# Optimization experiments

Hardware: AMD Instinct MI355X
Metric: run time of the kernel (lower is better)

The kernel has to match this reference:

```python
import jax, jax.numpy as jnp
import numpy as np

B, CIN, H, W = 4, 256, 128, 128   # x1/x2 each [B, CIN, H, W]
C2 = 2 * CIN                       # 512, channels after concat
CQK = CIN // 8                     # 32, query/key channels


def setup_inputs() -> dict:
    key = jax.random.key(0)
    ks = jax.random.split(key, 12)
    s = 0.02
    return {
        "x1": jax.random.normal(ks[0], (B, CIN, H, W), jnp.float32),
        "x2": jax.random.normal(ks[1], (B, CIN, H, W), jnp.float32),
        # 1x1 convs as [out,in] matrices + bias
        "Wq": jax.random.normal(ks[2], (CQK, C2), jnp.float32) * s,
        "bq": jnp.zeros((CQK,), jnp.float32),
        "Wk": jax.random.normal(ks[3], (CQK, C2), jnp.float32) * s,
        "bk": jnp.zeros((CQK,), jnp.float32),
        "Wv": jax.random.normal(ks[4], (C2, C2), jnp.float32) * s,
        "bv": jnp.zeros((C2,), jnp.float32),
        "Wm": jax.random.normal(ks[5], (C2, C2), jnp.float32) * s,
        "bm": jnp.zeros((C2,), jnp.float32),
        "gamma": jnp.zeros((1,), jnp.float32),
    }


def _conv1x1(w, b, x):
    # x: [b,c,h,w] -> [b,o,h,w]
    return jnp.einsum('oc,bchw->bohw', w, x) + b[None, :, None, None]


def reference(x1, x2, Wq, bq, Wk, bk, Wv, bv, Wm, bm, gamma):
    b, _, h, w = x1.shape
    x = jnp.concatenate([x1, x2], axis=1)          # [b, 2C, h, w]
    q = _conv1x1(Wq, bq, x)                        # [b, cqk, h, w]
    k = _conv1x1(Wk, bk, x)                        # [b, cqk, h, w]
    v = _conv1x1(Wv, bv, x)                        # [b, 2C, h, w]

    # column (H-axis) energy: [b, h_q, w, h_k], diagonal h_q==h_k masked to -inf
    energy_H = jnp.einsum('bciw,bcjw->biwj', q, k)
    diag = jnp.eye(h, dtype=bool)[None, :, None, :]
    energy_H = jnp.where(diag, -jnp.inf, energy_H)
    # row (W-axis) energy: [b, h, w_q, w_k]
    energy_W = jnp.einsum('bchi,bchj->bhij', q, k)

    concate = jax.nn.softmax(jnp.concatenate([energy_H, energy_W], axis=3), axis=3)
    att_H = concate[..., :h]                       # [b, h_q, w, h_k]
    att_W = concate[..., h:]                       # [b, h, w_q, w_k]

    out_H = jnp.einsum('bcjw,biwj->bciw', v, att_H)  # [b, 2C, h, w]
    out_W = jnp.einsum('bchj,bhij->bchi', v, att_W)  # [b, 2C, h, w]

    out = gamma[0] * (out_H + out_W) + x
    out = _conv1x1(Wm, bm, out)                    # [b, 2C, h, w]
    out = out.reshape(b, 2, C2 // 2, h, w).transpose(1, 0, 2, 3, 4)
    return out
```

## Files before the change

### kernel.cpp

```cpp
#include <hip/hip_runtime.h>
#include <cstdint>

#define HW 16384
#define HH 128
#define WW 128
#define C2 512
#define CQK 32
#define NB_TOT 4

typedef unsigned short u16;
typedef unsigned int u32;

using bf16x8 = __attribute__((ext_vector_type(8))) short;
using f32x4  = __attribute__((ext_vector_type(4))) float;

__device__ __forceinline__ float us2f(u16 u) { return __uint_as_float(((u32)u) << 16); }
__device__ __forceinline__ u16 f2us(float f) {
    u32 u = __float_as_uint(f);
    u = u + 0x7fffu + ((u >> 16) & 1u);
    return (u16)(u >> 16);
}
__device__ __forceinline__ u32 pack2(float a, float b) {
    return (u32)f2us(a) | ((u32)f2us(b) << 16);
}
__device__ __forceinline__ void unpack8(uint4 p, float* f) {
    u32 a[4] = {p.x, p.y, p.z, p.w};
#pragma unroll
    for (int q = 0; q < 4; ++q) {
        f[q * 2 + 0] = __uint_as_float(a[q] << 16);
        f[q * 2 + 1] = __uint_as_float(a[q] & 0xffff0000u);
    }
}
union U8 { uint4 v; u16 s[8]; };

__device__ __forceinline__ void gl_lds16(const void* g, const void* lds) {
    __builtin_amdgcn_global_load_lds(
        (const __attribute__((address_space(1))) unsigned int*)g,
        (__attribute__((address_space(3))) unsigned int*)lds, 16, 0, 0);
}

__global__ __launch_bounds__(256) void convert_weights(
    const float* __restrict__ Wq, const float* __restrict__ Wk,
    const float* __restrict__ Wv, const float* __restrict__ Wm,
    u16* __restrict__ Wall)
{
    int id = blockIdx.x * 256 + threadIdx.x;
    if (id >= 1088 * 128) return;
    int row = id >> 7, q4 = id & 127;
    const float* src;
    if (row < 32) src = Wq + (size_t)row * 512;
    else if (row < 64) src = Wk + (size_t)(row - 32) * 512;
    else if (row < 576) src = Wv + (size_t)(row - 64) * 512;
    else src = Wm + (size_t)(row - 576) * 512;
    float4 v = *reinterpret_cast<const float4*>(src + q4 * 4);
    alignas(8) u16 h[4] = {f2us(v.x), f2us(v.y), f2us(v.z), f2us(v.w)};
    *reinterpret_cast<uint2*>(Wall + (size_t)row * 512 + q4 * 4) =
        *reinterpret_cast<uint2*>(h);
}

__global__ __launch_bounds__(512) void conv_final(
    const u16* __restrict__ Wmb, const float* __restrict__ bm,
    const float* __restrict__ x1, const float* __restrict__ x2,
    const u16* __restrict__ y, float* __restrict__ out,
    int b0, const float* __restrict__ gamma)
{
    __shared__ u16 As[2][512 * 64];
    __shared__ u32 Ps[128 * 36];
    const int t = threadIdx.x, lane = t & 63, wid = t >> 6;
    const int bz = blockIdx.z, bg = b0 + bz;
    const int p0 = blockIdx.x * 128;
    const int l15 = lane & 15, l16 = lane >> 4;
    const bool useY = (gamma[0] != 0.f);
    const int pcol = t & 15, cpair = t >> 4;
    const u16* yb = y + (size_t)bz * C2 * HW;

    f32x4 acc[4][8];
#pragma unroll
    for (int i = 0; i < 4; ++i)
#pragma unroll
        for (int j = 0; j < 8; ++j) acc[i][j] = (f32x4)0.f;

    u32 xr[16];

    auto stageW = [&](int k0, int b) {
#pragma unroll
        for (int it = 0; it < 8; ++it) {
            int sflat = it * 512 + t;
            int m = sflat >> 3, slot = sflat & 7;
            int ck = slot ^ (m & 7);
            gl_lds16(Wmb + (size_t)m * 512 + k0 + ck * 8, &As[b][sflat * 8]);
        }
    };
    auto loadX = [&](int k0) {
        const int ce = k0 + cpair * 2;
        if (useY) {
            const u16* s0 = yb + (size_t)ce * HW + p0;
            const u16* s1 = s0 + HW;
#pragma unroll
            for (int i = 0; i < 8; ++i) {
                int p = pcol + i * 16;
                xr[i] = s0[p]; xr[8 + i] = s1[p];
            }
        } else {
            const float* s0 = (ce < 256) ? x1 + ((size_t)bg * 256 + ce) * HW + p0
                                         : x2 + ((size_t)bg * 256 + ce - 256) * HW + p0;
            const float* s1 = s0 + HW;
#pragma unroll
            for (int i = 0; i < 8; ++i) {
                int p = pcol + i * 16;
                xr[i] = __float_as_uint(s0[p]);
                xr[8 + i] = __float_as_uint(s1[p]);
            }
        }
    };
    auto writeX = [&]() {
#pragma unroll
        for (int i = 0; i < 8; ++i) {
            int p = pcol + i * 16;
            u32 d = useY ? (xr[i] | (xr[8 + i] << 16))
                         : pack2(__uint_as_float(xr[i]), __uint_as_float(xr[8 + i]));
            Ps[p * 36 + cpair] = d;
        }
    };

    stageW(0, 0);
    loadX(0);
    writeX();
    __syncthreads();

    for (int k = 0; k < 8; ++k) {
        const int cb = k & 1;
        if (k < 7) {
            stageW((k + 1) * 64, cb ^ 1);
            loadX((k + 1) * 64);
        }
#pragma unroll
        for (int kk = 0; kk < 2; ++kk) {
            bf16x8 af[4];
#pragma unroll
            for (int mi = 0; mi < 4; ++mi) {
                int row = wid * 64 + mi * 16 + l15;
                int slot = (kk * 4 + l16) ^ (row & 7);
                af[mi] = *(const bf16x8*)&As[cb][row * 64 + slot * 8];
            }
#pragma unroll
            for (int ni = 0; ni < 8; ++ni) {
                bf16x8 bq = *(const bf16x8*)((const u16*)&Ps[(ni * 16 + l15) * 36 + kk * 16 + l16 * 4]);
#pragma unroll
                for (int mi = 0; mi < 4; ++mi)
                    acc[mi][ni] = __builtin_amdgcn_mfma_f32_16x16x32_bf16(
                        af[mi], bq, acc[mi][ni], 0, 0, 0);
            }
        }
        __syncthreads();
        if (k < 7) {
            writeX();
            __syncthreads();
        }
    }
#pragma unroll
    for (int mi = 0; mi < 4; ++mi)
#pragma unroll
        for (int ni = 0; ni < 8; ++ni) {
            const int p = p0 + ni * 16 + l15;
#pragma unroll
            for (int r = 0; r < 4; ++r) {
                const int m = wid * 64 + mi * 16 + l16 * 4 + r;
                out[(((size_t)(m >> 8) * NB_TOT + bg) * 256 + (m & 255)) * HW + p] =
                    acc[mi][ni][r] + bm[m];
            }
        }
}

__global__ __launch_bounds__(256) void transpose_x(
    const float* __restrict__ x1, const float* __restrict__ x2,
    u16* __restrict__ xT, int b0, const float* __restrict__ gamma)
{
    if (gamma[0] == 0.f) return;
    __shared__ u16 tile[32][33];
    const int bz = blockIdx.z, bg = b0 + bz;
    const int p0 = blockIdx.x * 32;
    const int tx = threadIdx.x, ty = threadIdx.y;
    for (int cy = 0; cy < 16; ++cy) {
        const int c0 = cy * 32;
#pragma unroll
        for (int u = 0; u < 4; ++u) {
            int c = c0 + ty + u * 8;
            const float* xs = (c < 256) ? x1 + ((size_t)bg * 256 + c) * HW
                                        : x2 + ((size_t)bg * 256 + (c - 256)) * HW;
            tile[ty + u * 8][tx] = f2us(xs[p0 + tx]);
        }
        __syncthreads();
#pragma unroll
        for (int u = 0; u < 4; ++u) {
            int p = p0 + ty + u * 8;
            xT[((size_t)bz * HW + p) * 512 + c0 + tx] = tile[tx][ty + u * 8];
        }
        __syncthreads();
    }
}

template <int BM, int MODE>
__global__ __launch_bounds__(256) void conv_mfma(
    const u16* __restrict__ Wb, const float* __restrict__ bias0,
    const float* __restrict__ bias1, const u16* __restrict__ xT,
    float* __restrict__ oQ, float* __restrict__ oK,
    u16* __restrict__ oV, int b0, const float* __restrict__ gamma)
{
    if (gamma[0] == 0.f) return;
    constexpr int FM = BM / 32;
    __shared__ u16 As[BM * 64];
    __shared__ u16 Ps[128 * 64];
    const int t = threadIdx.x, lane = t & 63, wid = t >> 6;
    const int wr = wid >> 1, wc = wid & 1;
    const int bz = blockIdx.z;
    const int p0 = blockIdx.x * 128, m0 = blockIdx.y * BM;
    const u16* xTb = xT + (size_t)bz * HW * 512;
    const int l15 = lane & 15, l16 = lane >> 4;

    f32x4 acc[FM][4];
#pragma unroll
    for (int i = 0; i < FM; ++i)
#pragma unroll
        for (int j = 0; j < 4; ++j) acc[i][j] = (f32x4)0.f;

    for (int c0 = 0; c0 < 512; c0 += 64) {
#pragma unroll
        for (int it = 0; it < BM / 32; ++it) {
            int flat = it * 256 + t;
            int row = flat >> 3, part = flat & 7;
            gl_lds16(Wb + (size_t)(m0 + row) * 512 + c0 + part * 8,
                     As + (it * 256 + wid * 64) * 8);
        }
#pragma unroll
        for (int it = 0; it < 4; ++it) {
            int flat = it * 256 + t;
            int row = flat >> 3, part = flat & 7;
            gl_lds16(xTb + (size_t)(p0 + row) * 512 + c0 + part * 8,
                     Ps + (it * 256 + wid * 64) * 8);
        }
        __syncthreads();
#pragma unroll
        for (int kk = 0; kk < 2; ++kk) {
            bf16x8 af[FM], bfr[4];
#pragma unroll
            for (int mi = 0; mi < FM; ++mi)
                af[mi] = *(const bf16x8*)&As[(wr * (BM / 2) + mi * 16 + l15) * 64 + kk * 32 + l16 * 8];
#pragma unroll
            for (int ni = 0; ni < 4; ++ni)
                bfr[ni] = *(const bf16x8*)&Ps[(wc * 64 + ni * 16 + l15) * 64 + kk * 32 + l16 * 8];
#pragma unroll
            for (int mi = 0; mi < FM; ++mi)
#pragma unroll
                for (int ni = 0; ni < 4; ++ni)
                    acc[mi][ni] = __builtin_amdgcn_mfma_f32_16x16x32_bf16(
                        af[mi], bfr[ni], acc[mi][ni], 0, 0, 0);
        }
        __syncthreads();
    }
#pragma unroll
    for (int mi = 0; mi < FM; ++mi)
#pragma unroll
        for (int ni = 0; ni < 4; ++ni) {
            const int p = p0 + wc * 64 + ni * 16 + l15;
#pragma unroll
            for (int r = 0; r < 4; ++r) {
                const int m = m0 + wr * (BM / 2) + mi * 16 + l16 * 4 + r;
                float val = acc[mi][ni][r];
                if (MODE == 0) {
                    if (m < 32) {
                        val += bias0[m];
                        oQ[((size_t)bz * 32 + m) * HW + p] = val;
                    } else {
                        val += bias1[m - 32];
                        oK[((size_t)bz * 32 + (m - 32)) * HW + p] = val;
                    }
                } else {
                    val += bias0[m];
                    oV[((size_t)bz * 512 + m) * HW + p] = f2us(val);
                }
            }
        }
}

__global__ __launch_bounds__(256) void transpose_bf16(
    const u16* __restrict__ in, u16* __restrict__ out,
    const float* __restrict__ gamma)
{
    if (gamma[0] == 0.f) return;
    __shared__ u16 tile[32][33];
    const int x0 = blockIdx.x * 32, y0 = blockIdx.y * 32;
    const int tx = threadIdx.x, ty = threadIdx.y;
    for (int pp = 0; pp < 16; ++pp) {
        const int plane = blockIdx.z * 16 + pp;
        const u16* ip = in + (size_t)plane * HW;
        u16* op = out + (size_t)plane * HW;
#pragma unroll
        for (int u = 0; u < 4; ++u)
            tile[ty + u * 8][tx] = ip[(size_t)(y0 + ty + u * 8) * WW + x0 + tx];
        __syncthreads();
#pragma unroll
        for (int u = 0; u < 4; ++u)
            op[(size_t)(x0 + ty + u * 8) * HH + y0 + tx] = tile[tx][ty + u * 8];
        __syncthreads();
    }
}

__global__ __launch_bounds__(256) void energy_h_kernel(
    const float* __restrict__ q, const float* __restrict__ k,
    u16* __restrict__ EHt, const float* __restrict__ gamma)
{
    if (gamma[0] == 0.f) return;
    const int w = blockIdx.x, bz = blockIdx.y, t = threadIdx.x;
    __shared__ float qc[32][128];
    __shared__ float kc[32][128];
    __shared__ u16 es[128][128];
    for (int it = 0; it < 16; ++it) {
        int idx = it * 256 + t;
        int c = idx >> 7, j = idx & 127;
        qc[c][j] = q[((size_t)bz * CQK + c) * HW + j * WW + w];
        kc[c][j] = k[((size_t)bz * CQK + c) * HW + j * WW + w];
    }
    __syncthreads();
    const int i = t & 127, half = t >> 7, j0 = half * 64;
    float qi[32];
#pragma unroll
    for (int c = 0; c < 32; ++c) qi[c] = qc[c][i];
    for (int j = j0; j < j0 + 64; ++j) {
        float acc = 0.f;
#pragma unroll
        for (int c = 0; c < 32; ++c) acc += qi[c] * kc[c][j];
        es[i][j] = f2us(i == j ? -1e30f : acc);
    }
    __syncthreads();
    u16* dst = EHt + ((size_t)bz * WW + w) * HW;
    for (int it = 0; it < 8; ++it) {
        int ii = it * 16 + (t >> 4), jj = (t & 15) * 8;
        *reinterpret_cast<uint4*>(&dst[(size_t)ii * HH + jj]) =
            *reinterpret_cast<const uint4*>(&es[ii][jj]);
    }
}

__global__ __launch_bounds__(256) void ew_softmax_ow_kernel(
    const float* __restrict__ q, const float* __restrict__ k,
    const u16* __restrict__ v, u16* __restrict__ EHt,
    u16* __restrict__ oW, const float* __restrict__ gamma)
{
    if (gamma[0] == 0.f) return;
    const int r = blockIdx.x, bz = blockIdx.y, t = threadIdx.x;
    __shared__ float qr[32][128];
    __shared__ float kr[32][128];
    __shared__ u16 ewT[128][136];
    __shared__ u16 vstageT[128][40];
    __shared__ float invA[128];
    __shared__ float red[2][2][128];

    for (int it = 0; it < 16; ++it) {
        int idx = it * 256 + t, c = idx >> 7, j = idx & 127;
        qr[c][j] = q[((size_t)bz * CQK + c) * HW + r * WW + j];
        kr[c][j] = k[((size_t)bz * CQK + c) * HW + r * WW + j];
    }
    __syncthreads();
    const int i = t & 127, half = t >> 7, j0 = half * 64;
    {
        float qi[32];
#pragma unroll
        for (int c = 0; c < 32; ++c) qi[c] = qr[c][i];
        for (int j = j0; j < j0 + 64; ++j) {
            float acc = 0.f;
#pragma unroll
            for (int c = 0; c < 32; ++c) acc += qi[c] * kr[c][j];
            ewT[j][i] = f2us(acc);
        }
    }
    __syncthreads();
    float eh[64];
    u16* ehrow = EHt + (((size_t)bz * WW + i) * HH + r) * HH + j0;
#pragma unroll
    for (int uq = 0; uq < 8; ++uq) {
        uint4 pk = *reinterpret_cast<const uint4*>(ehrow + uq * 8);
        unpack8(pk, eh + uq * 8);
    }
    float m = -3e38f;
#pragma unroll
    for (int u = 0; u < 64; ++u) m = fmaxf(m, eh[u]);
    for (int j = j0; j < j0 + 64; ++j) m = fmaxf(m, us2f(ewT[j][i]));
    red[0][half][i] = m;
    __syncthreads();
    m = fmaxf(red[0][0][i], red[0][1][i]);
    float s = 0.f;
#pragma unroll
    for (int u = 0; u < 64; ++u) { float e = __expf(eh[u] - m); eh[u] = e; s += e; }
    for (int j = j0; j < j0 + 64; ++j) {
        float e = __expf(us2f(ewT[j][i]) - m);
        ewT[j][i] = f2us(e);
        s += e;
    }
    red[1][half][i] = s;
    __syncthreads();
    const float inv = 1.f / (red[1][0][i] + red[1][1][i]);
    if (half == 0) invA[i] = inv;
#pragma unroll
    for (int uq = 0; uq < 8; ++uq) {
        alignas(16) u16 tmp[8];
#pragma unroll
        for (int e = 0; e < 8; ++e) tmp[e] = f2us(eh[uq * 8 + e] * inv);
        *reinterpret_cast<uint4*>(ehrow + uq * 8) = *reinterpret_cast<uint4*>(tmp);
    }
    const int cg = half;
    for (int c0 = 0; c0 < C2; c0 += 32) {
        __syncthreads();
        for (int it = 0; it < 16; ++it) {
            int idx = it * 256 + t, cc = idx >> 7, j = idx & 127;
            vstageT[j][cc] = v[((size_t)bz * C2 + c0 + cc) * HW + r * WW + j];
        }
        __syncthreads();
        float acc[16] = {};
        for (int j = 0; j < 128; ++j) {
            float a = us2f(ewT[j][i]);
            uint4 pq0 = *reinterpret_cast<const uint4*>(&vstageT[j][cg * 16]);
            uint4 pq1 = *reinterpret_cast<const uint4*>(&vstageT[j][cg * 16 + 8]);
            float vv[16];
            unpack8(pq0, vv);
            unpack8(pq1, vv + 8);
#pragma unroll
            for (int u = 0; u < 16; ++u) acc[u] += a * vv[u];
        }
        const float scale = invA[i];
#pragma unroll
        for (int u = 0; u < 16; ++u) {
            int c = c0 + cg * 16 + u;
            oW[((size_t)bz * C2 + c) * HW + r * WW + i] = f2us(acc[u] * scale);
        }
    }
}

__global__ __launch_bounds__(256) void apply_h_kernel(
    const u16* __restrict__ EHt, const u16* __restrict__ vT,
    u16* __restrict__ oHT, const float* __restrict__ gamma)
{
    if (gamma[0] == 0.f) return;
    const int w = blockIdx.x, bz = blockIdx.y, t = threadIdx.x;
    __shared__ u16 aT[128][136];
    __shared__ u16 vstageT[128][40];
    const u16* src = EHt + ((size_t)bz * WW + w) * HW;
    for (int it = 0; it < 8; ++it) {
        int oct = it * 256 + t;
        int ii = oct >> 4, jj = (oct & 15) * 8;
        U8 uu;
        uu.v = *reinterpret_cast<const uint4*>(src + (size_t)ii * HH + jj);
#pragma unroll
        for (int e = 0; e < 8; ++e) aT[jj + e][ii] = uu.s[e];
    }
    const int i = t & 127, cg = t >> 7;
    for (int c0 = 0; c0 < C2; c0 += 32) {
        __syncthreads();
        for (int it = 0; it < 16; ++it) {
            int idx = it * 256 + t, cc = idx >> 7, j = idx & 127;
            vstageT[j][cc] = vT[((size_t)bz * C2 + c0 + cc) * HW + w * HH + j];
        }
        __syncthreads();
        float acc[16] = {};
        for (int j = 0; j < 128; ++j) {
            float a = us2f(aT[j][i]);
            uint4 pq0 = *reinterpret_cast<const uint4*>(&vstageT[j][cg * 16]);
            uint4 pq1 = *reinterpret_cast<const uint4*>(&vstageT[j][cg * 16 + 8]);
            float vv[16];
            unpack8(pq0, vv);
            unpack8(pq1, vv + 8);
#pragma unroll
            for (int u = 0; u < 16; ++u) acc[u] += a * vv[u];
        }
#pragma unroll
        for (int u = 0; u < 16; ++u) {
            int c = c0 + cg * 16 + u;
            oHT[((size_t)bz * C2 + c) * HW + w * HH + i] = f2us(acc[u]);
        }
    }
}

__global__ __launch_bounds__(256) void merge_transpose_kernel(
    const u16* __restrict__ oHT, const u16* __restrict__ oW,
    const float* __restrict__ x1, const float* __restrict__ x2,
    const float* __restrict__ gamma, u16* __restrict__ y, int b0)
{
    const float g = gamma[0];
    if (g == 0.f) return;
    __shared__ float tile[32][33];
    const int w0 = blockIdx.x * 32, i0 = blockIdx.y * 32;
    const int tx = threadIdx.x, ty = threadIdx.y;
    for (int pp = 0; pp < 16; ++pp) {
        const int idx = blockIdx.z * 16 + pp;
        const int c = idx & 511, bz = idx >> 9;
        const int bg = b0 + bz;
        const u16* ih = oHT + ((size_t)bz * C2 + c) * HW;
#pragma unroll
        for (int u = 0; u < 4; ++u)
            tile[ty + u * 8][tx] = us2f(ih[(size_t)(w0 + ty + u * 8) * HH + i0 + tx]);
        __syncthreads();
        const float* xs = (c < 256) ? (x1 + ((size_t)bg * 256 + c) * HW)
                                    : (x2 + ((size_t)bg * 256 + (c - 256)) * HW);
        const u16* ow = oW + ((size_t)bz * C2 + c) * HW;
        u16* yy = y + ((size_t)bz * C2 + c) * HW;
#pragma unroll
        for (int u = 0; u < 4; ++u) {
            int i = i0 + ty + u * 8, w = w0 + tx;
            float oh = tile[tx][ty + u * 8];
            float val = g * (oh + us2f(ow[(size_t)i * WW + w])) + xs[(size_t)i * WW + w];
            yy[(size_t)i * WW + w] = f2us(val);
        }
        __syncthreads();
    }
}

extern "C" void kernel_launch(void* const* d_in, const int* in_sizes, int n_in,
                              void* d_out, int out_size, void* d_ws, size_t ws_size,
                              hipStream_t stream)
{
    const float* x1 = (const float*)d_in[0];
    const float* x2 = (const float*)d_in[1];
    const float* Wq = (const float*)d_in[2];
    const float* bq = (const float*)d_in[3];
    const float* Wk = (const float*)d_in[4];
    const float* bk = (const float*)d_in[5];
    const float* Wv = (const float*)d_in[6];
    const float* bv = (const float*)d_in[7];
    const float* Wm = (const float*)d_in[8];
    const float* bm = (const float*)d_in[9];
    const float* gamma = (const float*)d_in[10];
    float* out = (float*)d_out;

    auto algn = [](size_t v) { return (v + 255) & ~(size_t)255; };
    const size_t wallSz = algn((size_t)1088 * 512 * 2);
    auto need = [&](int nb) -> size_t {
        size_t s = wallSz;
        s += algn((size_t)nb * HW * 512 * 2);
        s += 2 * algn((size_t)nb * 32 * HW * 4);
        s += algn((size_t)nb * C2 * HW * 2);
        s += algn((size_t)nb * C2 * HW * 2);
        s += algn((size_t)nb * WW * HW * 2);
        s += algn((size_t)nb * C2 * HW * 2);
        s += algn((size_t)nb * C2 * HW * 2);
        return s;
    };
    const int nb = (ws_size >= need(4)) ? 4 : (ws_size >= need(2)) ? 2 : 1;

    char* base = (char*)d_ws;
    u16* Wall = (u16*)base; base += wallSz;
    const u16* Wqk = Wall;
    const u16* Wvb = Wall + (size_t)64 * 512;
    const u16* Wmb = Wall + (size_t)576 * 512;

    convert_weights<<<(1088 * 128 + 255) / 256, 256, 0, stream>>>(Wq, Wk, Wv, Wm, Wall);

    for (int b0 = 0; b0 < NB_TOT; b0 += nb) {
        char* p = base;
        u16* xT   = (u16*)p;   p += algn((size_t)nb * HW * 512 * 2);
        float* q  = (float*)p; p += algn((size_t)nb * 32 * HW * 4);
        float* kk = (float*)p; p += algn((size_t)nb * 32 * HW * 4);
        u16* v    = (u16*)p;   p += algn((size_t)nb * C2 * HW * 2);
        u16* vT   = (u16*)p;   p += algn((size_t)nb * C2 * HW * 2);
        u16* EHt  = (u16*)p;   p += algn((size_t)nb * WW * HW * 2);
        u16* oW   = (u16*)p;   p += algn((size_t)nb * C2 * HW * 2);
        u16* oHT  = (u16*)p;   p += algn((size_t)nb * C2 * HW * 2);
        u16* y    = vT;

        transpose_x<<<dim3(HW / 32, 1, nb), dim3(32, 8), 0, stream>>>(
            x1, x2, xT, b0, gamma);
        conv_mfma<64, 0><<<dim3(HW / 128, 1, nb), 256, 0, stream>>>(
            Wqk, bq, bk, xT, q, kk, nullptr, b0, gamma);
        conv_mfma<128, 1><<<dim3(HW / 128, 4, nb), 256, 0, stream>>>(
            Wvb, bv, nullptr, xT, nullptr, nullptr, v, b0, gamma);
        transpose_bf16<<<dim3(4, 4, nb * 32), dim3(32, 8), 0, stream>>>(v, vT, gamma);
        energy_h_kernel<<<dim3(WW, nb), 256, 0, stream>>>(q, kk, EHt, gamma);
        ew_softmax_ow_kernel<<<dim3(HH, nb), 256, 0, stream>>>(q, kk, v, EHt, oW, gamma);
        apply_h_kernel<<<dim3(WW, nb), 256, 0, stream>>>(EHt, vT, oHT, gamma);
        merge_transpose_kernel<<<dim3(4, 4, nb * 32), dim3(32, 8), 0, stream>>>(
            oHT, oW, x1, x2, gamma, y, b0);
        conv_final<<<dim3(HW / 128, 1, nb), 512, 0, stream>>>(
            Wmb, bm, x1, x2, y, out, b0, gamma);
    }
}
```

Before: 87.62 us.

## Vectorize conv_final X loads, relax barrier, skip unused weight conversion when gamma is zero

conv_final's X loader now maps 32 lanes to channel pairs and 8 lanes to pixel groups, so each thread issues 16-byte vector loads instead of scattered scalar loads. The X load is issued before the weight staging, and the trailing __syncthreads is replaced by a raw s_barrier plus sched_barrier, so the outstanding global loads are not drained before the LDS write. convert_weights skips converting Wq/Wk/Wv when gamma is zero, because the attention branch is not consumed then. The relaxed barrier depends on the LDS write being ordered correctly without a full waitcnt, and the gamma skip depends on downstream kernels also bypassing those weights.

Result: slower. 109.9 us (+25.4%).

```diff
diff --git a/kernel.cpp b/kernel.cpp
--- a/kernel.cpp
+++ b/kernel.cpp
@@ -42,11 +42,12 @@
 __global__ __launch_bounds__(256) void convert_weights(
     const float* __restrict__ Wq, const float* __restrict__ Wk,
     const float* __restrict__ Wv, const float* __restrict__ Wm,
-    u16* __restrict__ Wall)
+    u16* __restrict__ Wall, const float* __restrict__ gamma)
 {
     int id = blockIdx.x * 256 + threadIdx.x;
     if (id >= 1088 * 128) return;
     int row = id >> 7, q4 = id & 127;
+    if (row < 576 && gamma[0] == 0.f) return;
     const float* src;
     if (row < 32) src = Wq + (size_t)row * 512;
     else if (row < 64) src = Wk + (size_t)(row - 32) * 512;
@@ -71,7 +72,8 @@
     const int p0 = blockIdx.x * 128;
     const int l15 = lane & 15, l16 = lane >> 4;
     const bool useY = (gamma[0] != 0.f);
-    const int pcol = t & 15, cpair = t >> 4;
+    const int cpair = t & 31;
+    const int pgroup = t >> 5;
     const u16* yb = y + (size_t)bz * C2 * HW;
 
     f32x4 acc[4][8];
@@ -82,6 +84,45 @@
 
     u32 xr[16];
 
+    auto loadX = [&](int k0) {
+        const int ce = k0 + cpair * 2;
+        if (useY) {
+            const u16* s0 = yb + (size_t)ce * HW + p0 + pgroup * 8;
+            uint4 h0 = *reinterpret_cast<const uint4*>(s0);
+            uint4 h1 = *reinterpret_cast<const uint4*>(s0 + HW);
+            xr[0] = h0.x; xr[1] = h0.y; xr[2] = h0.z; xr[3] = h0.w;
+            xr[8] = h1.x; xr[9] = h1.y; xr[10] = h1.z; xr[11] = h1.w;
+        } else {
+            const float* s0 = (ce < 256) ? x1 + ((size_t)bg * 256 + ce) * HW + p0 + pgroup * 8
+                                         : x2 + ((size_t)bg * 256 + ce - 256) * HW + p0 + pgroup * 8;
+            float4 a0 = *reinterpret_cast<const float4*>(s0);
+            float4 a1 = *reinterpret_cast<const float4*>(s0 + 4);
+            float4 b0v = *reinterpret_cast<const float4*>(s0 + HW);
+            float4 b1v = *reinterpret_cast<const float4*>(s0 + HW + 4);
+            xr[0] = __float_as_uint(a0.x); xr[1] = __float_as_uint(a0.y);
+            xr[2] = __float_as_uint(a0.z); xr[3] = __float_as_uint(a0.w);
+            xr[4] = __float_as_uint(a1.x); xr[5] = __float_as_uint(a1.y);
+            xr[6] = __float_as_uint(a1.z); xr[7] = __float_as_uint(a1.w);
+            xr[8] = __float_as_uint(b0v.x); xr[9] = __float_as_uint(b0v.y);
+            xr[10] = __float_as_uint(b0v.z); xr[11] = __float_as_uint(b0v.w);
+            xr[12] = __float_as_uint(b1v.x); xr[13] = __float_as_uint(b1v.y);
+            xr[14] = __float_as_uint(b1v.z); xr[15] = __float_as_uint(b1v.w);
+        }
+    };
+    auto writeX = [&]() {
+#pragma unroll
+        for (int i = 0; i < 8; ++i) {
+            u32 d;
+            if (useY) {
+                u32 lo = (xr[i >> 1] >> ((i & 1) * 16)) & 0xffffu;
+                u32 hi = (xr[8 + (i >> 1)] >> ((i & 1) * 16)) & 0xffffu;
+                d = lo | (hi << 16);
+            } else {
+                d = pack2(__uint_as_float(xr[i]), __uint_as_float(xr[8 + i]));
+            }
+            Ps[(pgroup * 8 + i) * 36 + cpair] = d;
+        }
+    };
     auto stageW = [&](int k0, int b) {
 #pragma unroll
         for (int it = 0; it < 8; ++it) {
@@ -91,48 +132,17 @@
             gl_lds16(Wmb + (size_t)m * 512 + k0 + ck * 8, &As[b][sflat * 8]);
         }
     };
-    auto loadX = [&](int k0) {
-        const int ce = k0 + cpair * 2;
-        if (useY) {
-            const u16* s0 = yb + (size_t)ce * HW + p0;
-            const u16* s1 = s0 + HW;
-#pragma unroll
-            for (int i = 0; i < 8; ++i) {
-                int p = pcol + i * 16;
-                xr[i] = s0[p]; xr[8 + i] = s1[p];
-            }
-        } else {
-            const float* s0 = (ce < 256) ? x1 + ((size_t)bg * 256 + ce) * HW + p0
-                                         : x2 + ((size_t)bg * 256 + ce - 256) * HW + p0;
-            const float* s1 = s0 + HW;
-#pragma unroll
-            for (int i = 0; i < 8; ++i) {
-                int p = pcol + i * 16;
-                xr[i] = __float_as_uint(s0[p]);
-                xr[8 + i] = __float_as_uint(s1[p]);
-            }
-        }
-    };
-    auto writeX = [&]() {
-#pragma unroll
-        for (int i = 0; i < 8; ++i) {
-            int p = pcol + i * 16;
-            u32 d = useY ? (xr[i] | (xr[8 + i] << 16))
-                         : pack2(__uint_as_float(xr[i]), __uint_as_float(xr[8 + i]));
-            Ps[p * 36 + cpair] = d;
-        }
-    };
-
+
+    loadX(0);
     stageW(0, 0);
-    loadX(0);
     writeX();
     __syncthreads();
 
     for (int k = 0; k < 8; ++k) {
         const int cb = k & 1;
         if (k < 7) {
+            loadX((k + 1) * 64);
             stageW((k + 1) * 64, cb ^ 1);
-            loadX((k + 1) * 64);
         }
 #pragma unroll
         for (int kk = 0; kk < 2; ++kk) {
@@ -152,8 +162,9 @@
                         af[mi], bq, acc[mi][ni], 0, 0, 0);
             }
         }
-        __syncthreads();
         if (k < 7) {
+            __builtin_amdgcn_s_barrier();
+            __builtin_amdgcn_sched_barrier(0);
             writeX();
             __syncthreads();
         }
@@ -551,7 +562,8 @@
     const u16* Wvb = Wall + (size_t)64 * 512;
     const u16* Wmb = Wall + (size_t)576 * 512;
 
-    convert_weights<<<(1088 * 128 + 255) / 256, 256, 0, stream>>>(Wq, Wk, Wv, Wm, Wall);
+    convert_weights<<<(1088 * 128 + 255) / 256, 256, 0, stream>>>(
+        Wq, Wk, Wv, Wm, Wall, gamma);
 
     for (int b0 = 0; b0 < NB_TOT; b0 += nb) {
         char* p = base;
```
